# Kernel optimization log

Measured on AMD Instinct MI355X. Metric: run time of the kernel, lower is better.

Reference implementation:

```python
import jax, jax.numpy as jnp
import numpy as np

N_NODES = 50000
N_EDGES = 400000
NODE_DIM = 128
NUM_BASIS = 20
MUL0, MUL1, MUL2 = 128, 64, 32          # 128x0e + 64x1e + 32x2e
NUM_IRREPS = MUL0 + MUL1 + MUL2         # 224
SPH_DIM = MUL0 + 3 * MUL1 + 5 * MUL2    # 480
HIDDEN = NODE_DIM + NUM_IRREPS          # 352
EPS = 1e-5


def layer_norm(x, g, b):
    mu = x.mean(-1, keepdims=True)
    var = ((x - mu) ** 2).mean(-1, keepdims=True)
    return (x - mu) * jax.lax.rsqrt(var + EPS) * g + b


def o3_layer_norm(x, w, b):
    # Equivariant layer norm per irrep block (Equiformer-style, component normalization).
    s = x[:, :MUL0]                                    # l=0 scalars [N,128]
    v = x[:, MUL0:MUL0 + 3 * MUL1].reshape(-1, MUL1, 3)  # l=1 [N,64,3]
    t = x[:, MUL0 + 3 * MUL1:].reshape(-1, MUL2, 5)      # l=2 [N,32,5]
    s = s - s.mean(-1, keepdims=True)
    s = s * jax.lax.rsqrt((s ** 2).mean(-1, keepdims=True) + EPS) * w[:MUL0] + b
    nv = (v ** 2).mean(axis=(-1, -2))[:, None, None]
    v = v * jax.lax.rsqrt(nv + EPS) * w[MUL0:MUL0 + MUL1][None, :, None]
    nt = (t ** 2).mean(axis=(-1, -2))[:, None, None]
    t = t * jax.lax.rsqrt(nt + EPS) * w[MUL0 + MUL1:][None, :, None]
    return jnp.concatenate([s, v.reshape(-1, 3 * MUL1), t.reshape(-1, 5 * MUL2)], axis=-1)


def sph_harm(vec):
    # e3nn spherical harmonics (normalize=True, normalization='component') up to l=2.
    u = vec * jax.lax.rsqrt((vec ** 2).sum(-1, keepdims=True))
    x, y, z = u[:, 0], u[:, 1], u[:, 2]
    s15 = np.float32(np.sqrt(15.0))
    s5 = np.float32(np.sqrt(5.0))
    sh1 = np.float32(np.sqrt(3.0)) * u  # [E,3]
    sh2 = jnp.stack([s15 * x * z,
                     s15 * x * y,
                     s5 * (y * y - 0.5 * (x * x + z * z)),
                     s15 * y * z,
                     0.5 * s15 * (z * z - x * x)], axis=-1)  # [E,5]
    return sh1, sh2


def _forward(x_scalar, x_spherical, rbf, vec, W1, b1, W2, b2, Wrbf, ln_g, ln_b, o3_w, o3_b, edge_index):
    dst, src = edge_index[0], edge_index[1]
    scalar_in = layer_norm(x_scalar, ln_g, ln_b)          # [N,128]
    spherical_in = o3_layer_norm(x_spherical, o3_w, o3_b)  # [N,480]
    h = jax.nn.silu(scalar_in @ W1 + b1)
    scalar_out = h @ W2 + b2                               # [N,352]
    filter_weight = rbf @ Wrbf                             # [E,352]
    filter_out = scalar_out[src] * filter_weight           # gather + elementwise [E,352]
    gate = filter_out[:, :NUM_IRREPS]                      # [E,224]
    message_scalar = filter_out[:, NUM_IRREPS:]            # [E,128]
    sh1, sh2 = sph_harm(vec)
    g0 = gate[:, :MUL0]
    g1 = gate[:, MUL0:MUL0 + MUL1]
    g2 = gate[:, MUL0 + MUL1:]
    # ElementwiseTensorProduct(edge_irreps, '224x0e'): scalar gate per irrep; l=0 SH == 1.
    msg1 = (g1[:, :, None] * sh1[:, None, :]).reshape(-1, 3 * MUL1)
    msg2 = (g2[:, :, None] * sh2[:, None, :]).reshape(-1, 5 * MUL2)
    message_spherical = jnp.concatenate([g0, msg1, msg2], axis=-1)  # [E,480]
    new_scalar = scalar_in.at[dst].add(message_scalar)
    new_spherical = spherical_in.at[dst].add(message_spherical)
    return new_scalar, new_spherical


def setup_inputs() -> dict:
    key = jax.random.key(0)
    ks = jax.random.split(key, 8)
    return {
        "x_scalar": jax.random.normal(ks[0], (N_NODES, NODE_DIM), dtype=jnp.float32),
        "x_spherical": jax.random.normal(ks[1], (N_NODES, SPH_DIM), dtype=jnp.float32),
        "rbf": jax.random.normal(ks[2], (N_EDGES, NUM_BASIS), dtype=jnp.float32),
        "vec": jax.random.normal(ks[3], (N_EDGES, 3), dtype=jnp.float32),
        "W1": jax.random.normal(ks[4], (NODE_DIM, NODE_DIM), dtype=jnp.float32) * 0.05,
        "b1": jnp.zeros((NODE_DIM,), jnp.float32),
        "W2": jax.random.normal(ks[5], (NODE_DIM, HIDDEN), dtype=jnp.float32) * 0.05,
        "b2": jnp.zeros((HIDDEN,), jnp.float32),
        "Wrbf": jax.random.normal(ks[6], (NUM_BASIS, HIDDEN), dtype=jnp.float32) * 0.05,
        "ln_g": jnp.ones((NODE_DIM,), jnp.float32),
        "ln_b": jnp.zeros((NODE_DIM,), jnp.float32),
        "o3_w": jnp.ones((NUM_IRREPS,), jnp.float32),
        "o3_b": jnp.zeros((MUL0,), jnp.float32),
        "edge_index": jax.random.randint(ks[7], (2, N_EDGES), 0, N_NODES),
    }


def reference(x_scalar, x_spherical, rbf, vec, W1, b1, W2, b2, Wrbf, ln_g, ln_b, o3_w, o3_b, edge_index):
    return _forward(x_scalar, x_spherical, rbf, vec, W1, b1, W2, b2, Wrbf, ln_g, ln_b, o3_w, o3_b, edge_index)
```

## Files before the change

kernel.cpp:

```cpp
#include <hip/hip_runtime.h>
#include <hip/hip_bf16.h>

#define N_DIM   128
#define MUL0    128
#define MUL1    64
#define MUL2    32
#define NIRR    224
#define SPHD    480
#define HID     352
#define NBASIS  20
#define EPSV    1e-5f

typedef __attribute__((ext_vector_type(8))) short bf16x8;
typedef __attribute__((ext_vector_type(4))) float f32x4;

__device__ __forceinline__ float wave_sum(float v) {
  #pragma unroll
  for (int o = 32; o > 0; o >>= 1) v += __shfl_xor(v, o, 64);
  return v;
}

__device__ __forceinline__ unsigned short f2bf(float f) {
  unsigned int u = __float_as_uint(f);
  u = (u + 0x7fff + ((u >> 16) & 1)) >> 16;
  return (unsigned short)u;
}

__device__ __forceinline__ float bf2f(unsigned short v) {
  return __uint_as_float(((unsigned int)v) << 16);
}

__global__ __launch_bounds__(256) void node_norm_kernel(
    const float* __restrict__ x_scalar, const float* __restrict__ x_sph,
    const float* __restrict__ ln_g, const float* __restrict__ ln_b,
    const float* __restrict__ o3_w, const float* __restrict__ o3_b,
    float* __restrict__ out_scal, float* __restrict__ out_sph, int n_nodes) {
  const int n = blockIdx.x * 4 + (threadIdx.x >> 6);
  if (n >= n_nodes) return;
  const int l = threadIdx.x & 63;

  const float* xs = x_scalar + (size_t)n * N_DIM;
  float a0 = xs[l], a1 = xs[l + 64];
  float mu = wave_sum(a0 + a1) * (1.f / 128.f);
  float d0 = a0 - mu, d1 = a1 - mu;
  float var = wave_sum(d0 * d0 + d1 * d1) * (1.f / 128.f);
  float sc = rsqrtf(var + EPSV);
  float* os = out_scal + (size_t)n * N_DIM;
  os[l]      = d0 * sc * ln_g[l]      + ln_b[l];
  os[l + 64] = d1 * sc * ln_g[l + 64] + ln_b[l + 64];

  const float* xp = x_sph + (size_t)n * SPHD;
  float s0 = xp[l], s1 = xp[l + 64];
  mu = wave_sum(s0 + s1) * (1.f / 128.f);
  d0 = s0 - mu; d1 = s1 - mu;
  var = wave_sum(d0 * d0 + d1 * d1) * (1.f / 128.f);
  sc = rsqrtf(var + EPSV);
  float* op = out_sph + (size_t)n * SPHD;
  op[l]      = d0 * sc * o3_w[l]      + o3_b[l];
  op[l + 64] = d1 * sc * o3_w[l + 64] + o3_b[l + 64];

  float v0 = xp[128 + l], v1 = xp[128 + 64 + l], v2 = xp[128 + 128 + l];
  float nv = wave_sum(v0 * v0 + v1 * v1 + v2 * v2) * (1.f / 192.f);
  sc = rsqrtf(nv + EPSV);
  op[128 + l]       = v0 * sc * o3_w[MUL0 + (l) / 3];
  op[128 + 64 + l]  = v1 * sc * o3_w[MUL0 + (l + 64) / 3];
  op[128 + 128 + l] = v2 * sc * o3_w[MUL0 + (l + 128) / 3];

  float t0 = xp[320 + l], t1 = xp[320 + 64 + l];
  float t2 = (l < 32) ? xp[320 + 128 + l] : 0.f;
  float nt = wave_sum(t0 * t0 + t1 * t1 + t2 * t2) * (1.f / 160.f);
  sc = rsqrtf(nt + EPSV);
  op[320 + l]      = t0 * sc * o3_w[MUL0 + MUL1 + (l) / 5];
  op[320 + 64 + l] = t1 * sc * o3_w[MUL0 + MUL1 + (l + 64) / 5];
  if (l < 32) op[320 + 128 + l] = t2 * sc * o3_w[MUL0 + MUL1 + (l + 128) / 5];
}

__global__ void pack_b_kernel(const float* __restrict__ B, unsigned short* __restrict__ Bp,
                              int N, int NT) {
  int id = blockIdx.x * 256 + threadIdx.x;
  int total = 4 * NT * 64;
  if (id >= total) return;
  int lane = id & 63;
  int tmp = id >> 6;
  int nt = tmp % NT, ks = tmp / NT;
  int n = nt * 16 + (lane & 15);
  int kb = ks * 32 + (lane >> 4) * 8;
  unsigned short* o = Bp + (size_t)id * 8;
  #pragma unroll
  for (int j = 0; j < 8; ++j)
    o[j] = (n < N) ? f2bf(B[(size_t)(kb + j) * N + n]) : (unsigned short)0;
}

template <bool A_BF16, bool SILU, bool OUT_BF16, bool PERM>
__global__ __launch_bounds__(256) void mfma_gemm_kernel(
    const void* __restrict__ Ap, const unsigned short* __restrict__ Bp,
    const float* __restrict__ bias, void* __restrict__ Cp,
    int M, int N, int NT) {
  const int lane = threadIdx.x & 63;
  const int wave = threadIdx.x >> 6;
  const int bm = blockIdx.x * 64 + wave * 16;
  const int bn = blockIdx.y * 64;
  const int q = lane >> 4;
  const int arow = min(bm + (lane & 15), M - 1);

  f32x4 acc[4] = {};
  #pragma unroll
  for (int ks = 0; ks < 4; ++ks) {
    const int k = ks * 32 + q * 8;
    bf16x8 a;
    if (A_BF16) {
      a = *(const bf16x8*)((const unsigned short*)Ap + (size_t)arow * 128 + k);
    } else {
      const float* ap = (const float*)Ap + (size_t)arow * 128 + k;
      float4 f0 = *(const float4*)ap;
      float4 f1 = *(const float4*)(ap + 4);
      union { bf16x8 v; unsigned short s[8]; } cv;
      cv.s[0] = f2bf(f0.x); cv.s[1] = f2bf(f0.y); cv.s[2] = f2bf(f0.z); cv.s[3] = f2bf(f0.w);
      cv.s[4] = f2bf(f1.x); cv.s[5] = f2bf(f1.y); cv.s[6] = f2bf(f1.z); cv.s[7] = f2bf(f1.w);
      a = cv.v;
    }
    #pragma unroll
    for (int nt = 0; nt < 4; ++nt) {
      bf16x8 b = *(const bf16x8*)(Bp + ((size_t)(ks * NT + blockIdx.y * 4 + nt) * 64 + lane) * 8);
      acc[nt] = __builtin_amdgcn_mfma_f32_16x16x32_bf16(a, b, acc[nt], 0, 0, 0);
    }
  }
  #pragma unroll
  for (int nt = 0; nt < 4; ++nt) {
    int col = bn + nt * 16 + (lane & 15);
    if (col >= N) continue;
    float bz = bias[col];
    int pcol = col;
    if (PERM) pcol = (col < 96) ? (2 * col) : ((col < 256) ? (col + 96) : (2 * (col - 256) + 1));
    #pragma unroll
    for (int i = 0; i < 4; ++i) {
      int r = bm + q * 4 + i;
      if (r >= M) continue;
      float v = acc[nt][i] + bz;
      if (SILU) v = v / (1.f + __expf(-v));
      if (OUT_BF16) ((unsigned short*)Cp)[(size_t)r * N + pcol] = f2bf(v);
      else          ((float*)Cp)[(size_t)r * N + pcol] = v;
    }
  }
}

__global__ void hist_kernel(const int* __restrict__ ei, int* __restrict__ deg, int n_edges) {
  int e = blockIdx.x * blockDim.x + threadIdx.x;
  if (e < n_edges) atomicAdd(&deg[ei[e]], 1);
}

__global__ __launch_bounds__(1024) void scan_part_kernel(
    const int* __restrict__ deg, int* __restrict__ offs, int* __restrict__ bsum, int n) {
  __shared__ int wsum[16];
  const int tid = threadIdx.x, lane = tid & 63, wid = tid >> 6;
  int i = blockIdx.x * 1024 + tid;
  int v = (i < n) ? deg[i] : 0;
  int s = v;
  #pragma unroll
  for (int o = 1; o < 64; o <<= 1) {
    int t = __shfl_up(s, o, 64);
    if (lane >= o) s += t;
  }
  if (lane == 63) wsum[wid] = s;
  __syncthreads();
  if (wid == 0) {
    int ws = (lane < 16) ? wsum[lane] : 0;
    #pragma unroll
    for (int o = 1; o < 16; o <<= 1) {
      int t = __shfl_up(ws, o, 64);
      if (lane >= o) ws += t;
    }
    if (lane < 16) wsum[lane] = ws;
  }
  __syncthreads();
  int excl = ((wid == 0) ? 0 : wsum[wid - 1]) + s - v;
  if (i < n) offs[i] = excl;
  if (tid == 1023) bsum[blockIdx.x] = wsum[15];
}

__global__ __launch_bounds__(64) void scan_tops_kernel(
    const int* __restrict__ bsum, int* __restrict__ bbase, int* __restrict__ offs,
    int nb, int n) {
  const int lane = threadIdx.x;
  int v = (lane < nb) ? bsum[lane] : 0;
  int s = v;
  #pragma unroll
  for (int o = 1; o < 64; o <<= 1) {
    int t = __shfl_up(s, o, 64);
    if (lane >= o) s += t;
  }
  if (lane < nb) bbase[lane] = s - v;
  if (lane == 63) offs[n] = s;
}

__global__ __launch_bounds__(1024) void scan_add_kernel(
    int* __restrict__ offs, const int* __restrict__ bbase, int n) {
  int i = blockIdx.x * 1024 + threadIdx.x;
  if (i < n) offs[i] += bbase[blockIdx.x];
}

__global__ void fill_kernel(const int* __restrict__ ei, const int* __restrict__ offs,
                            int* __restrict__ cursor, const int* __restrict__ edge_src,
                            const float* __restrict__ rbf, const float* __restrict__ vec,
                            float* __restrict__ rbf_s, float* __restrict__ vec_s,
                            int* __restrict__ src_s, int n_edges) {
  int e = blockIdx.x * blockDim.x + threadIdx.x;
  if (e < n_edges) {
    int d = ei[e];
    int p = atomicAdd(&cursor[d], 1);
    int ii = offs[d] + p;
    src_s[ii] = edge_src[e];
    const float4* rp = (const float4*)(rbf + (size_t)e * NBASIS);
    float4* op = (float4*)(rbf_s + (size_t)ii * NBASIS);
    op[0] = rp[0]; op[1] = rp[1]; op[2] = rp[2]; op[3] = rp[3]; op[4] = rp[4];
    vec_s[(size_t)ii * 3]     = vec[(size_t)e * 3];
    vec_s[(size_t)ii * 3 + 1] = vec[(size_t)e * 3 + 1];
    vec_s[(size_t)ii * 3 + 2] = vec[(size_t)e * 3 + 2];
  }
}

#define NPB 4
#define S3f  1.7320508075688772f
#define S15f 3.872983346207417f
#define S5f  2.2360679774997896f

__device__ __forceinline__ void so_load(const unsigned short* __restrict__ so,
                                        int src, int t, bool hasB,
                                        float& sA, float& sB) {
  const unsigned short* p = so + (size_t)src * HID;
  if (hasB) {
    unsigned int u = *(const unsigned int*)(p + 2 * t);
    sA = __uint_as_float(u << 16);
    sB = __uint_as_float(u & 0xffff0000u);
  } else {
    sA = bf2f(p[t + 96]);
    sB = 0.f;
  }
}

__device__ __forceinline__ void edge_accum(
    int ii, float sA, float sB,
    const float* __restrict__ rbf_s, const float* __restrict__ vec_s,
    const float* wA, const float* wB, int t, bool hasB,
    float& a0, float& a1, float& a2, float& a3, float& a4, float& aB) {
  const float4* rp = (const float4*)(rbf_s + (size_t)ii * NBASIS);
  float4 r0 = rp[0], r1 = rp[1], r2 = rp[2], r3 = rp[3], r4 = rp[4];
  float rb[NBASIS] = {r0.x, r0.y, r0.z, r0.w, r1.x, r1.y, r1.z, r1.w,
                      r2.x, r2.y, r2.z, r2.w, r3.x, r3.y, r3.z, r3.w,
                      r4.x, r4.y, r4.z, r4.w};
  float fwA = 0.f;
  #pragma unroll
  for (int k = 0; k < NBASIS; ++k) fwA += rb[k] * wA[k];
  float fA = sA * fwA;

  if (t < 128) {
    a0 += fA;
  } else if (t < 224) {
    float vx = vec_s[3 * (size_t)ii], vy = vec_s[3 * (size_t)ii + 1], vz = vec_s[3 * (size_t)ii + 2];
    float rn = rsqrtf(vx * vx + vy * vy + vz * vz);
    float x = vx * rn, y = vy * rn, z = vz * rn;
    if (t < 192) {
      a0 += fA * (S3f * x); a1 += fA * (S3f * y); a2 += fA * (S3f * z);
    } else {
      a0 += fA * (S15f * x * z);
      a1 += fA * (S15f * x * y);
      a2 += fA * (S5f * (y * y - 0.5f * (x * x + z * z)));
      a3 += fA * (S15f * y * z);
      a4 += fA * (0.5f * S15f * (z * z - x * x));
    }
  } else {
    a0 += fA;
  }

  if (hasB) {
    float fwB = 0.f;
    #pragma unroll
    for (int k = 0; k < NBASIS; ++k) fwB += rb[k] * wB[k];
    aB += sB * fwB;
  }
}

__global__ __launch_bounds__(256) void gather_kernel(
    const float* __restrict__ rbf_s, const float* __restrict__ vec_s,
    const float* __restrict__ Wrbf, const unsigned short* __restrict__ so,
    const int* __restrict__ src_s, const int* __restrict__ offs,
    float* __restrict__ out_scal, float* __restrict__ out_sph, int n_nodes) {
  const int t = threadIdx.x;
  const bool hasB = (t < 96);
  const int cA = t;
  const int cB = hasB ? (256 + t) : 256;

  float wA[NBASIS], wB[NBASIS];
  #pragma unroll
  for (int k = 0; k < NBASIS; ++k) {
    wA[k] = Wrbf[k * HID + cA];
    wB[k] = Wrbf[k * HID + cB];
  }

  const int nb = blockIdx.x * NPB;
  for (int nn = 0; nn < NPB; ++nn) {
    const int node = nb + nn;
    if (node >= n_nodes) break;
    float a0 = 0.f, a1 = 0.f, a2 = 0.f, a3 = 0.f, a4 = 0.f, aB = 0.f;
    const int e0 = offs[node], e1 = offs[node + 1];

    int ii = e0;
    for (; ii + 4 <= e1; ii += 4) {
      const int s0 = src_s[ii], s1 = src_s[ii + 1], s2 = src_s[ii + 2], s3 = src_s[ii + 3];
      float sA0, sB0, sA1, sB1, sA2, sB2, sA3, sB3;
      so_load(so, s0, t, hasB, sA0, sB0);
      so_load(so, s1, t, hasB, sA1, sB1);
      so_load(so, s2, t, hasB, sA2, sB2);
      so_load(so, s3, t, hasB, sA3, sB3);
      edge_accum(ii,     sA0, sB0, rbf_s, vec_s, wA, wB, t, hasB, a0, a1, a2, a3, a4, aB);
      edge_accum(ii + 1, sA1, sB1, rbf_s, vec_s, wA, wB, t, hasB, a0, a1, a2, a3, a4, aB);
      edge_accum(ii + 2, sA2, sB2, rbf_s, vec_s, wA, wB, t, hasB, a0, a1, a2, a3, a4, aB);
      edge_accum(ii + 3, sA3, sB3, rbf_s, vec_s, wA, wB, t, hasB, a0, a1, a2, a3, a4, aB);
    }
    for (; ii + 2 <= e1; ii += 2) {
      const int s0 = src_s[ii], s1 = src_s[ii + 1];
      float sA0, sB0, sA1, sB1;
      so_load(so, s0, t, hasB, sA0, sB0);
      so_load(so, s1, t, hasB, sA1, sB1);
      edge_accum(ii,     sA0, sB0, rbf_s, vec_s, wA, wB, t, hasB, a0, a1, a2, a3, a4, aB);
      edge_accum(ii + 1, sA1, sB1, rbf_s, vec_s, wA, wB, t, hasB, a0, a1, a2, a3, a4, aB);
    }
    if (ii < e1) {
      const int s0 = src_s[ii];
      float sA0, sB0;
      so_load(so, s0, t, hasB, sA0, sB0);
      edge_accum(ii, sA0, sB0, rbf_s, vec_s, wA, wB, t, hasB, a0, a1, a2, a3, a4, aB);
    }

    float* sph = out_sph + (size_t)node * SPHD;
    float* scl = out_scal + (size_t)node * N_DIM;
    if (t < 128) {
      sph[t] += a0;
    } else if (t < 192) {
      float* p = sph + 128 + 3 * (t - 128);
      p[0] += a0; p[1] += a1; p[2] += a2;
    } else if (t < 224) {
      float* p = sph + 320 + 5 * (t - 192);
      p[0] += a0; p[1] += a1; p[2] += a2; p[3] += a3; p[4] += a4;
    } else {
      scl[t - 224] += a0;
    }
    if (hasB) scl[t + 32] += aB;
  }
}

extern "C" void kernel_launch(void* const* d_in, const int* in_sizes, int n_in,
                              void* d_out, int out_size, void* d_ws, size_t ws_size,
                              hipStream_t stream) {
  const float* x_scalar = (const float*)d_in[0];
  const float* x_sph    = (const float*)d_in[1];
  const float* rbf      = (const float*)d_in[2];
  const float* vec      = (const float*)d_in[3];
  const float* W1       = (const float*)d_in[4];
  const float* b1       = (const float*)d_in[5];
  const float* W2       = (const float*)d_in[6];
  const float* b2       = (const float*)d_in[7];
  const float* Wrbf     = (const float*)d_in[8];
  const float* ln_g     = (const float*)d_in[9];
  const float* ln_b     = (const float*)d_in[10];
  const float* o3_w     = (const float*)d_in[11];
  const float* o3_b     = (const float*)d_in[12];
  const int*   edge_idx = (const int*)d_in[13];

  const int n_nodes = in_sizes[0] / N_DIM;
  const int n_edges = in_sizes[2] / NBASIS;

  float* out_scal = (float*)d_out;
  float* out_sph  = out_scal + (size_t)n_nodes * N_DIM;

  float* rbf_s = (float*)d_ws;
  float* vec_s = rbf_s + (size_t)n_edges * NBASIS;
  int*   src_s = (int*)(vec_s + (size_t)n_edges * 3);
  unsigned short* so_bf = (unsigned short*)(src_s + n_edges);
  unsigned short* h_bf  = so_bf + (size_t)n_nodes * HID;
  unsigned short* bp1   = h_bf + (size_t)n_nodes * N_DIM;
  unsigned short* bp2   = bp1 + 16384;
  int* deg    = (int*)(bp2 + 49152);
  int* cursor = deg + n_nodes;
  int* offs   = cursor + n_nodes;
  int* bsum   = offs + n_nodes + 1;
  int* bbase  = bsum + 64;

  const int* edge_dst = edge_idx;
  const int* edge_src = edge_idx + n_edges;

  node_norm_kernel<<<(n_nodes + 3) / 4, 256, 0, stream>>>(
      x_scalar, x_sph, ln_g, ln_b, o3_w, o3_b, out_scal, out_sph, n_nodes);

  pack_b_kernel<<<8, 256, 0, stream>>>(W1, bp1, N_DIM, 8);
  pack_b_kernel<<<24, 256, 0, stream>>>(W2, bp2, HID, 24);

  {
    dim3 g((n_nodes + 63) / 64, 2);
    mfma_gemm_kernel<false, true, true, false><<<g, 256, 0, stream>>>(
        out_scal, bp1, b1, h_bf, n_nodes, N_DIM, 8);
  }
  {
    dim3 g((n_nodes + 63) / 64, 6);
    mfma_gemm_kernel<true, false, true, true><<<g, 256, 0, stream>>>(
        h_bf, bp2, b2, so_bf, n_nodes, HID, 24);
  }

  hipMemsetAsync(deg, 0, sizeof(int) * 2 * n_nodes, stream);
  hist_kernel<<<(n_edges + 255) / 256, 256, 0, stream>>>(edge_dst, deg, n_edges);
  const int nb = (n_nodes + 1023) / 1024;
  scan_part_kernel<<<nb, 1024, 0, stream>>>(deg, offs, bsum, n_nodes);
  scan_tops_kernel<<<1, 64, 0, stream>>>(bsum, bbase, offs, nb, n_nodes);
  scan_add_kernel<<<nb, 1024, 0, stream>>>(offs, bbase, n_nodes);
  fill_kernel<<<(n_edges + 255) / 256, 256, 0, stream>>>(
      edge_dst, offs, cursor, edge_src, rbf, vec, rbf_s, vec_s, src_s, n_edges);

  gather_kernel<<<(n_nodes + NPB - 1) / NPB, 256, 0, stream>>>(
      rbf_s, vec_s, Wrbf, so_bf, src_s, offs, out_scal, out_sph, n_nodes);
}
```

Baseline: 679.8 us.

## Stage per-block edge rbf and spherical harmonics in LDS for gather

The gather kernel now loads each block's contiguous edge range in chunks into shared memory: rbf rows, source indices, and spherical harmonics computed once per edge rather than once per thread. Wrbf is transposed into a workspace so each thread loads its 20 weights as vector loads, and the launch bounds request higher occupancy. This removes redundant per-thread global loads and repeated rsqrt/harmonic math. The cost is extra block barriers, shared-memory traffic, and a small extra pack kernel.

```diff
diff --git a/kernel.cpp b/kernel.cpp
--- a/kernel.cpp
+++ b/kernel.cpp
@@ -89,6 +89,13 @@
   #pragma unroll
   for (int j = 0; j < 8; ++j)
     o[j] = (n < N) ? f2bf(B[(size_t)(kb + j) * N + n]) : (unsigned short)0;
+}
+
+__global__ void pack_wt_kernel(const float* __restrict__ Wrbf, float* __restrict__ Wt) {
+  int id = blockIdx.x * 256 + threadIdx.x;
+  if (id >= HID * NBASIS) return;
+  int c = id / NBASIS, k = id - c * NBASIS;
+  Wt[id] = Wrbf[k * HID + c];
 }
 
 template <bool A_BF16, bool SILU, bool OUT_BF16, bool PERM>
@@ -220,6 +227,7 @@
 }
 
 #define NPB 4
+#define CHUNK 64
 #define S3f  1.7320508075688772f
 #define S15f 3.872983346207417f
 #define S5f  2.2360679774997896f
@@ -238,114 +246,145 @@
   }
 }
 
-__device__ __forceinline__ void edge_accum(
-    int ii, float sA, float sB,
+__global__ __launch_bounds__(256, 4) void gather_kernel(
     const float* __restrict__ rbf_s, const float* __restrict__ vec_s,
-    const float* wA, const float* wB, int t, bool hasB,
-    float& a0, float& a1, float& a2, float& a3, float& a4, float& aB) {
-  const float4* rp = (const float4*)(rbf_s + (size_t)ii * NBASIS);
-  float4 r0 = rp[0], r1 = rp[1], r2 = rp[2], r3 = rp[3], r4 = rp[4];
-  float rb[NBASIS] = {r0.x, r0.y, r0.z, r0.w, r1.x, r1.y, r1.z, r1.w,
-                      r2.x, r2.y, r2.z, r2.w, r3.x, r3.y, r3.z, r3.w,
-                      r4.x, r4.y, r4.z, r4.w};
-  float fwA = 0.f;
-  #pragma unroll
-  for (int k = 0; k < NBASIS; ++k) fwA += rb[k] * wA[k];
-  float fA = sA * fwA;
-
-  if (t < 128) {
-    a0 += fA;
-  } else if (t < 224) {
-    float vx = vec_s[3 * (size_t)ii], vy = vec_s[3 * (size_t)ii + 1], vz = vec_s[3 * (size_t)ii + 2];
-    float rn = rsqrtf(vx * vx + vy * vy + vz * vz);
-    float x = vx * rn, y = vy * rn, z = vz * rn;
-    if (t < 192) {
-      a0 += fA * (S3f * x); a1 += fA * (S3f * y); a2 += fA * (S3f * z);
-    } else {
-      a0 += fA * (S15f * x * z);
-      a1 += fA * (S15f * x * y);
-      a2 += fA * (S5f * (y * y - 0.5f * (x * x + z * z)));
-      a3 += fA * (S15f * y * z);
-      a4 += fA * (0.5f * S15f * (z * z - x * x));
-    }
-  } else {
-    a0 += fA;
-  }
-
-  if (hasB) {
-    float fwB = 0.f;
-    #pragma unroll
-    for (int k = 0; k < NBASIS; ++k) fwB += rb[k] * wB[k];
-    aB += sB * fwB;
-  }
-}
-
-__global__ __launch_bounds__(256) void gather_kernel(
-    const float* __restrict__ rbf_s, const float* __restrict__ vec_s,
-    const float* __restrict__ Wrbf, const unsigned short* __restrict__ so,
+    const float* __restrict__ Wt, const unsigned short* __restrict__ so,
     const int* __restrict__ src_s, const int* __restrict__ offs,
     float* __restrict__ out_scal, float* __restrict__ out_sph, int n_nodes) {
+  __shared__ float rbf_l[CHUNK * NBASIS];
+  __shared__ float sh_l[CHUNK * 8];
+  __shared__ int   src_l[CHUNK];
+
   const int t = threadIdx.x;
   const bool hasB = (t < 96);
-  const int cA = t;
-  const int cB = hasB ? (256 + t) : 256;
-
-  float wA[NBASIS], wB[NBASIS];
-  #pragma unroll
-  for (int k = 0; k < NBASIS; ++k) {
-    wA[k] = Wrbf[k * HID + cA];
-    wB[k] = Wrbf[k * HID + cB];
-  }
-
-  const int nb = blockIdx.x * NPB;
+
+  const f32x4* wap = (const f32x4*)(Wt + (size_t)t * NBASIS);
+  f32x4 wA0 = wap[0], wA1 = wap[1], wA2 = wap[2], wA3 = wap[3], wA4 = wap[4];
+  const f32x4* wbp = (const f32x4*)(Wt + (size_t)(hasB ? (256 + t) : 256) * NBASIS);
+  f32x4 wB0 = wbp[0], wB1 = wbp[1], wB2 = wbp[2], wB3 = wbp[3], wB4 = wbp[4];
+  asm volatile("" : "+v"(wA0), "+v"(wA1), "+v"(wA2), "+v"(wA3), "+v"(wA4));
+  asm volatile("" : "+v"(wB0), "+v"(wB1), "+v"(wB2), "+v"(wB3), "+v"(wB4));
+
+  const int n0 = blockIdx.x * NPB;
+  if (n0 >= n_nodes) return;
+  const int nE = min(n0 + NPB, n_nodes);
+  const int E0 = offs[n0], E1 = offs[nE];
+
+  int eb0[NPB], eb1[NPB];
+  #pragma unroll
+  for (int i = 0; i < NPB; ++i) {
+    int nd = n0 + i;
+    eb0[i] = (nd < n_nodes) ? offs[nd] : E1;
+    eb1[i] = (nd < n_nodes) ? offs[nd + 1] : E1;
+  }
+
+  float a0[NPB] = {}, a1[NPB] = {}, a2[NPB] = {}, a3[NPB] = {}, a4[NPB] = {}, aB[NPB] = {};
+
+  for (int C0 = E0; C0 < E1; C0 += CHUNK) {
+    const int C1 = min(C0 + CHUNK, E1);
+    const int ns = C1 - C0;
+
+    for (int i = t; i < ns * NBASIS; i += 256)
+      rbf_l[i] = rbf_s[(size_t)C0 * NBASIS + i];
+    if (t < ns) {
+      const int ii = C0 + t;
+      src_l[t] = src_s[ii];
+      float vx = vec_s[3 * (size_t)ii], vy = vec_s[3 * (size_t)ii + 1], vz = vec_s[3 * (size_t)ii + 2];
+      float rn = rsqrtf(vx * vx + vy * vy + vz * vz);
+      float x = vx * rn, y = vy * rn, z = vz * rn;
+      float* sp = &sh_l[t * 8];
+      sp[0] = S3f * x; sp[1] = S3f * y; sp[2] = S3f * z;
+      sp[3] = S15f * x * z;
+      sp[4] = S15f * x * y;
+      sp[5] = S5f * (y * y - 0.5f * (x * x + z * z));
+      sp[6] = S15f * y * z;
+      sp[7] = 0.5f * S15f * (z * z - x * x);
+    }
+    __syncthreads();
+
+    auto edge = [&](int il, float sA, float sB, int nn) {
+      const float* rbp = &rbf_l[il * NBASIS];
+      f32x4 r0 = *(const f32x4*)(rbp);
+      f32x4 r1 = *(const f32x4*)(rbp + 4);
+      f32x4 r2 = *(const f32x4*)(rbp + 8);
+      f32x4 r3 = *(const f32x4*)(rbp + 12);
+      f32x4 r4 = *(const f32x4*)(rbp + 16);
+      float fwA = 0.f;
+      fwA += r0[0] * wA0[0]; fwA += r0[1] * wA0[1]; fwA += r0[2] * wA0[2]; fwA += r0[3] * wA0[3];
+      fwA += r1[0] * wA1[0]; fwA += r1[1] * wA1[1]; fwA += r1[2] * wA1[2]; fwA += r1[3] * wA1[3];
+      fwA += r2[0] * wA2[0]; fwA += r2[1] * wA2[1]; fwA += r2[2] * wA2[2]; fwA += r2[3] * wA2[3];
+      fwA += r3[0] * wA3[0]; fwA += r3[1] * wA3[1]; fwA += r3[2] * wA3[2]; fwA += r3[3] * wA3[3];
+      fwA += r4[0] * wA4[0]; fwA += r4[1] * wA4[1]; fwA += r4[2] * wA4[2]; fwA += r4[3] * wA4[3];
+      float fA = sA * fwA;
+
+      if (t < 128) {
+        a0[nn] += fA;
+      } else if (t < 224) {
+        const float* sp = &sh_l[il * 8];
+        if (t < 192) {
+          a0[nn] += fA * sp[0]; a1[nn] += fA * sp[1]; a2[nn] += fA * sp[2];
+        } else {
+          a0[nn] += fA * sp[3]; a1[nn] += fA * sp[4]; a2[nn] += fA * sp[5];
+          a3[nn] += fA * sp[6]; a4[nn] += fA * sp[7];
+        }
+      } else {
+        a0[nn] += fA;
+      }
+
+      if (hasB) {
+        float fwB = 0.f;
+        fwB += r0[0] * wB0[0]; fwB += r0[1] * wB0[1]; fwB += r0[2] * wB0[2]; fwB += r0[3] * wB0[3];
+        fwB += r1[0] * wB1[0]; fwB += r1[1] * wB1[1]; fwB += r1[2] * wB1[2]; fwB += r1[3] * wB1[3];
+        fwB += r2[0] * wB2[0]; fwB += r2[1] * wB2[1]; fwB += r2[2] * wB2[2]; fwB += r2[3] * wB2[3];
+        fwB += r3[0] * wB3[0]; fwB += r3[1] * wB3[1]; fwB += r3[2] * wB3[2]; fwB += r3[3] * wB3[3];
+        fwB += r4[0] * wB4[0]; fwB += r4[1] * wB4[1]; fwB += r4[2] * wB4[2]; fwB += r4[3] * wB4[3];
+        aB[nn] += sB * fwB;
+      }
+    };
+
+    #pragma unroll
+    for (int nn = 0; nn < NPB; ++nn) {
+      const int lo = max(eb0[nn], C0);
+      const int hi = min(eb1[nn], C1);
+      int ii = lo;
+      for (; ii + 2 <= hi; ii += 2) {
+        const int il0 = ii - C0, il1 = il0 + 1;
+        const int s0 = src_l[il0], s1 = src_l[il1];
+        float sA0, sB0, sA1, sB1;
+        so_load(so, s0, t, hasB, sA0, sB0);
+        so_load(so, s1, t, hasB, sA1, sB1);
+        edge(il0, sA0, sB0, nn);
+        edge(il1, sA1, sB1, nn);
+      }
+      if (ii < hi) {
+        const int il0 = ii - C0;
+        const int s0 = src_l[il0];
+        float sA0, sB0;
+        so_load(so, s0, t, hasB, sA0, sB0);
+        edge(il0, sA0, sB0, nn);
+      }
+    }
+    __syncthreads();
+  }
+
+  #pragma unroll
   for (int nn = 0; nn < NPB; ++nn) {
-    const int node = nb + nn;
+    const int node = n0 + nn;
     if (node >= n_nodes) break;
-    float a0 = 0.f, a1 = 0.f, a2 = 0.f, a3 = 0.f, a4 = 0.f, aB = 0.f;
-    const int e0 = offs[node], e1 = offs[node + 1];
-
-    int ii = e0;
-    for (; ii + 4 <= e1; ii += 4) {
-      const int s0 = src_s[ii], s1 = src_s[ii + 1], s2 = src_s[ii + 2], s3 = src_s[ii + 3];
-      float sA0, sB0, sA1, sB1, sA2, sB2, sA3, sB3;
-      so_load(so, s0, t, hasB, sA0, sB0);
-      so_load(so, s1, t, hasB, sA1, sB1);
-      so_load(so, s2, t, hasB, sA2, sB2);
-      so_load(so, s3, t, hasB, sA3, sB3);
-      edge_accum(ii,     sA0, sB0, rbf_s, vec_s, wA, wB, t, hasB, a0, a1, a2, a3, a4, aB);
-      edge_accum(ii + 1, sA1, sB1, rbf_s, vec_s, wA, wB, t, hasB, a0, a1, a2, a3, a4, aB);
-      edge_accum(ii + 2, sA2, sB2, rbf_s, vec_s, wA, wB, t, hasB, a0, a1, a2, a3, a4, aB);
-      edge_accum(ii + 3, sA3, sB3, rbf_s, vec_s, wA, wB, t, hasB, a0, a1, a2, a3, a4, aB);
-    }
-    for (; ii + 2 <= e1; ii += 2) {
-      const int s0 = src_s[ii], s1 = src_s[ii + 1];
-      float sA0, sB0, sA1, sB1;
-      so_load(so, s0, t, hasB, sA0, sB0);
-      so_load(so, s1, t, hasB, sA1, sB1);
-      edge_accum(ii,     sA0, sB0, rbf_s, vec_s, wA, wB, t, hasB, a0, a1, a2, a3, a4, aB);
-      edge_accum(ii + 1, sA1, sB1, rbf_s, vec_s, wA, wB, t, hasB, a0, a1, a2, a3, a4, aB);
-    }
-    if (ii < e1) {
-      const int s0 = src_s[ii];
-      float sA0, sB0;
-      so_load(so, s0, t, hasB, sA0, sB0);
-      edge_accum(ii, sA0, sB0, rbf_s, vec_s, wA, wB, t, hasB, a0, a1, a2, a3, a4, aB);
-    }
-
     float* sph = out_sph + (size_t)node * SPHD;
     float* scl = out_scal + (size_t)node * N_DIM;
     if (t < 128) {
-      sph[t] += a0;
+      sph[t] += a0[nn];
     } else if (t < 192) {
       float* p = sph + 128 + 3 * (t - 128);
-      p[0] += a0; p[1] += a1; p[2] += a2;
+      p[0] += a0[nn]; p[1] += a1[nn]; p[2] += a2[nn];
     } else if (t < 224) {
       float* p = sph + 320 + 5 * (t - 192);
-      p[0] += a0; p[1] += a1; p[2] += a2; p[3] += a3; p[4] += a4;
+      p[0] += a0[nn]; p[1] += a1[nn]; p[2] += a2[nn]; p[3] += a3[nn]; p[4] += a4[nn];
     } else {
-      scl[t - 224] += a0;
-    }
-    if (hasB) scl[t + 32] += aB;
+      scl[t - 224] += a0[nn];
+    }
+    if (hasB) scl[t + 32] += aB[nn];
   }
 }
 
@@ -385,6 +424,7 @@
   int* offs   = cursor + n_nodes;
   int* bsum   = offs + n_nodes + 1;
   int* bbase  = bsum + 64;
+  float* Wt   = (float*)(bbase + 64);
 
   const int* edge_dst = edge_idx;
   const int* edge_src = edge_idx + n_edges;
@@ -394,6 +434,7 @@
 
   pack_b_kernel<<<8, 256, 0, stream>>>(W1, bp1, N_DIM, 8);
   pack_b_kernel<<<24, 256, 0, stream>>>(W2, bp2, HID, 24);
+  pack_wt_kernel<<<(HID * NBASIS + 255) / 256, 256, 0, stream>>>(Wrbf, Wt);
 
   {
     dim3 g((n_nodes + 63) / 64, 2);
@@ -416,5 +457,5 @@
       edge_dst, offs, cursor, edge_src, rbf, vec, rbf_s, vec_s, src_s, n_edges);
 
   gather_kernel<<<(n_nodes + NPB - 1) / NPB, 256, 0, stream>>>(
-      rbf_s, vec_s, Wrbf, so_bf, src_s, offs, out_scal, out_sph, n_nodes);
-}
+      rbf_s, vec_s, Wt, so_bf, src_s, offs, out_scal, out_sph, n_nodes);
+}
```

After: 698.7 us. +2.8%, slower.
